# Kernel optimization log

Hardware: AMD Instinct MI355X
Metric: run time of the kernel (lower is better)

## Reference

```python
import jax, jax.numpy as jnp
import numpy as np

B, S, H, NH = 2, 2048, 768, 12
HD = H // NH  # 64
MAXPOS = 2048


def _rope_tables(max_pos, d):
    # bert4torch get_sinusoid_encoding_table: even cols sin, odd cols cos
    pos = np.arange(max_pos, dtype=np.float32)[:, None]
    div = np.exp(np.arange(0, d, 2, dtype=np.float32) * (-np.log(10000.0) / d))
    tab = np.zeros((max_pos, d), np.float32)
    tab[:, 0::2] = np.sin(pos * div)
    tab[:, 1::2] = np.cos(pos * div)
    cos = np.concatenate([tab[:, 1::2], tab[:, 1::2]], axis=1)  # [:,1::2].repeat(1,2)
    sin = np.concatenate([tab[:, 0::2], tab[:, 0::2]], axis=1)  # [:,0::2].repeat(1,2)
    return jnp.asarray(cos), jnp.asarray(sin)


def setup_inputs() -> dict:
    key = jax.random.key(0)
    ks = jax.random.split(key, 10)
    s = 0.02
    inp = {}
    inp["hidden_states"] = jax.random.normal(ks[0], (B, S, H), jnp.float32)
    inp["attention_mask"] = jnp.ones((B, 1, 1, S), jnp.float32)
    for i, n in enumerate(["q", "k", "v", "o"]):
        inp[f"W{n}"] = (jax.random.normal(ks[1 + i], (H, H), jnp.float32) * s)
        inp[f"b{n}"] = jnp.zeros((H,), jnp.float32)
    cos, sin = _rope_tables(MAXPOS, HD)
    inp["cos_position"] = cos
    inp["sin_position"] = sin
    return inp


def _apply_rope(qw, cos, sin):
    # Faithful to source: seq_len_dim defaults to 1, which on a
    # [B, heads, S, head_dim] tensor is the HEADS axis.
    L = qw.shape[1]
    qw2 = jnp.concatenate([-qw[..., 1::2], qw[..., 0::2]], axis=-1)
    return qw * cos[:L][None, :, None, :] + qw2 * sin[:L][None, :, None, :]


def reference(hidden_states, attention_mask, Wq, bq, Wk, bk, Wv, bv, Wo, bo,
              cos_position, sin_position):
    b, s, _ = hidden_states.shape

    def heads(x):  # [b,s,H] -> [b,NH,s,HD]
        return x.reshape(b, s, NH, HD).transpose(0, 2, 1, 3)

    q = heads(hidden_states @ Wq + bq)
    k = heads(hidden_states @ Wk + bk)
    v = heads(hidden_states @ Wv + bv)
    q = _apply_rope(q, cos_position, sin_position)
    k = _apply_rope(k, cos_position, sin_position)
    scores = jnp.einsum('bnid,bnjd->bnij', q, k) / jnp.sqrt(jnp.float32(HD))
    scores = scores + (1.0 - attention_mask) * (-10000.0)
    probs = jax.nn.softmax(scores, axis=-1)  # dropout is identity in eval
    ctx = jnp.einsum('bnij,bnjd->bnid', probs, v)
    ctx = ctx.transpose(0, 2, 1, 3).reshape(b, s, H)
    return ctx @ Wo + bo
```

## Files before the change

kernel.cpp:

```cpp
#include <hip/hip_runtime.h>

#define B 2
#define S 2048
#define H 768
#define NH 12
#define HD 64
#define BS (B * S)
#define LOG2E 1.4426950408889634f

typedef unsigned short u16;
typedef short short8 __attribute__((ext_vector_type(8)));
typedef float f32x4 __attribute__((ext_vector_type(4)));
typedef float f32x16 __attribute__((ext_vector_type(16)));

__device__ __forceinline__ u16 f2bf(float f) {
    union { float f; unsigned u; } c; c.f = f;
    unsigned u = c.u + 0x7FFFu + ((c.u >> 16) & 1u);
    return (u16)(u >> 16);
}
__device__ __forceinline__ float bf2f(u16 h) {
    union { unsigned u; float f; } c; c.u = ((unsigned)h) << 16;
    return c.f;
}
__device__ __forceinline__ f32x16 zero16() {
    f32x16 v;
    #pragma unroll
    for (int i = 0; i < 16; ++i) v[i] = 0.f;
    return v;
}

__device__ __forceinline__ void g2l16(const u16* g, u16* l) {
    __builtin_amdgcn_global_load_lds(
        (const __attribute__((address_space(1))) void*)g,
        (__attribute__((address_space(3))) void*)l, 16, 0, 0);
}

__global__ __launch_bounds__(256) void prep_hs_kernel(
    const float* __restrict__ src, u16* __restrict__ dst)
{
    size_t i = ((size_t)blockIdx.x * 256 + threadIdx.x) * 8;
    float4 a = *(const float4*)(src + i);
    float4 b = *(const float4*)(src + i + 4);
    short8 p;
    p[0] = (short)f2bf(a.x); p[1] = (short)f2bf(a.y);
    p[2] = (short)f2bf(a.z); p[3] = (short)f2bf(a.w);
    p[4] = (short)f2bf(b.x); p[5] = (short)f2bf(b.y);
    p[6] = (short)f2bf(b.z); p[7] = (short)f2bf(b.w);
    *(short8*)(dst + i) = p;
}

__global__ __launch_bounds__(256) void prep_w_kernel(
    const float* __restrict__ Wq, const float* __restrict__ Wk,
    const float* __restrict__ Wv, const float* __restrict__ Wo,
    u16* __restrict__ WTqkv, u16* __restrict__ WTo)
{
    __shared__ float Lt[64 * 65];
    const int t = threadIdx.x;
    const int z = blockIdx.z;
    const float* W = (z == 0) ? Wq : (z == 1) ? Wk : (z == 2) ? Wv : Wo;
    u16* D = (z == 3) ? WTo : (WTqkv + (size_t)z * H * H);
    const int k0 = blockIdx.x * 64, n0 = blockIdx.y * 64;

    #pragma unroll
    for (int u = 0; u < 4; ++u) {
        int f = t + u * 256;
        int r = f >> 4, c4 = (f & 15) * 4;
        float4 w = *(const float4*)(W + (size_t)(k0 + r) * H + n0 + c4);
        Lt[r * 65 + c4 + 0] = w.x; Lt[r * 65 + c4 + 1] = w.y;
        Lt[r * 65 + c4 + 2] = w.z; Lt[r * 65 + c4 + 3] = w.w;
    }
    __syncthreads();
    #pragma unroll
    for (int u = 0; u < 4; ++u) {
        int f = t + u * 256;
        int n = f >> 4, k4 = (f & 15) * 4;
        ushort4 p;
        p.x = f2bf(Lt[(k4 + 0) * 65 + n]);
        p.y = f2bf(Lt[(k4 + 1) * 65 + n]);
        p.z = f2bf(Lt[(k4 + 2) * 65 + n]);
        p.w = f2bf(Lt[(k4 + 3) * 65 + n]);
        *(ushort4*)(D + (size_t)(n0 + n) * H + k0 + k4) = p;
    }
}

__global__ __launch_bounds__(256) void gemm_qkv_kernel(
    const u16* __restrict__ A, const u16* __restrict__ BT,
    const float* __restrict__ bq, const float* __restrict__ bk,
    const float* __restrict__ bv,
    u16* __restrict__ Qb, u16* __restrict__ Kb, u16* __restrict__ VT)
{
    __shared__ alignas(16) u16 As[128 * 72];
    __shared__ alignas(16) u16 Bs[128 * 72];

    const int tid  = threadIdx.x;
    const int w    = tid >> 6;
    const int lane = tid & 63;
    const int quad = lane >> 4;
    const int l15  = lane & 15;
    const int wm = (w & 1) * 64, wn = (w >> 1) * 64;
    const int m0 = blockIdx.x * 128;
    const int n0 = blockIdx.y * 128;
    const int lr = tid >> 3, lc8 = (tid & 7) * 8;

    f32x4 acc[4][4];
    #pragma unroll
    for (int i = 0; i < 4; ++i)
        #pragma unroll
        for (int j = 0; j < 4; ++j) acc[i][j] = (f32x4){0.f, 0.f, 0.f, 0.f};

    short8 pa[2], pb[2], pa2[2], pb2[2];
    #pragma unroll
    for (int u = 0; u < 2; ++u) {
        pa[u]  = *(const short8*)(A  + (size_t)(m0 + lr + u * 32) * H + lc8);
        pb[u]  = *(const short8*)(BT + (size_t)(n0 + lr + u * 32) * H + lc8);
        pa2[u] = *(const short8*)(A  + (size_t)(m0 + lr + 64 + u * 32) * H + lc8);
        pb2[u] = *(const short8*)(BT + (size_t)(n0 + lr + 64 + u * 32) * H + lc8);
    }

    for (int k0 = 0; k0 < H; k0 += 64) {
        __syncthreads();
        #pragma unroll
        for (int u = 0; u < 2; ++u) {
            *(short8*)&As[(lr + u * 32) * 72 + lc8] = pa[u];
            *(short8*)&Bs[(lr + u * 32) * 72 + lc8] = pb[u];
            *(short8*)&As[(lr + 64 + u * 32) * 72 + lc8] = pa2[u];
            *(short8*)&Bs[(lr + 64 + u * 32) * 72 + lc8] = pb2[u];
        }
        if (k0 + 64 < H) {
            #pragma unroll
            for (int u = 0; u < 2; ++u) {
                pa[u]  = *(const short8*)(A  + (size_t)(m0 + lr + u * 32) * H + k0 + 64 + lc8);
                pb[u]  = *(const short8*)(BT + (size_t)(n0 + lr + u * 32) * H + k0 + 64 + lc8);
                pa2[u] = *(const short8*)(A  + (size_t)(m0 + lr + 64 + u * 32) * H + k0 + 64 + lc8);
                pb2[u] = *(const short8*)(BT + (size_t)(n0 + lr + 64 + u * 32) * H + k0 + 64 + lc8);
            }
        }
        __syncthreads();
        #pragma unroll
        for (int kc = 0; kc < 64; kc += 32) {
            short8 af[4], bf[4];
            #pragma unroll
            for (int mi = 0; mi < 4; ++mi)
                af[mi] = *(const short8*)&As[(wm + mi * 16 + l15) * 72 + kc + quad * 8];
            #pragma unroll
            for (int ni = 0; ni < 4; ++ni)
                bf[ni] = *(const short8*)&Bs[(wn + ni * 16 + l15) * 72 + kc + quad * 8];
            #pragma unroll
            for (int mi = 0; mi < 4; ++mi)
                #pragma unroll
                for (int ni = 0; ni < 4; ++ni)
                    acc[mi][ni] = __builtin_amdgcn_mfma_f32_16x16x32_bf16(
                        af[mi], bf[ni], acc[mi][ni], 0, 0, 0);
        }
    }

    #pragma unroll
    for (int mi = 0; mi < 4; ++mi) {
        const int mbase = m0 + wm + mi * 16 + quad * 4;
        #pragma unroll
        for (int ni = 0; ni < 4; ++ni) {
            const int col = n0 + wn + ni * 16 + l15;
            const int which = col / H;
            const int c = col - which * H;
            const int h = c >> 6, d = c & 63;
            if (which == 2) {
                const float bias = bv[c];
                const int b_ = mbase >> 11, s = mbase & (S - 1);
                ushort4 pk;
                pk.x = f2bf(acc[mi][ni][0] + bias);
                pk.y = f2bf(acc[mi][ni][1] + bias);
                pk.z = f2bf(acc[mi][ni][2] + bias);
                pk.w = f2bf(acc[mi][ni][3] + bias);
                *(ushort4*)&VT[(((size_t)b_ * NH + h) * HD + d) * S + s] = pk;
            } else {
                u16* dst = (which == 0) ? Qb : Kb;
                const float bias = (which == 0) ? bq[c] : bk[c];
                #pragma unroll
                for (int r = 0; r < 4; ++r) {
                    int m = mbase + r;
                    int b_ = m >> 11, s = m & (S - 1);
                    dst[(((size_t)b_ * NH + h) * S + s) * HD + d] =
                        f2bf(acc[mi][ni][r] + bias);
                }
            }
        }
    }
}

__global__ __launch_bounds__(256) void gemm_out_kernel(
    const u16* __restrict__ A, const u16* __restrict__ BT,
    const float* __restrict__ bo, float* __restrict__ out)
{
    __shared__ alignas(16) u16 As[128 * 72];
    __shared__ alignas(16) u16 Bs[64 * 72];

    const int tid  = threadIdx.x;
    const int w    = tid >> 6;
    const int lane = tid & 63;
    const int quad = lane >> 4;
    const int l15  = lane & 15;
    const int wm = (w & 1) * 64, wn = (w >> 1) * 32;
    const int m0 = blockIdx.x * 128;
    const int n0 = blockIdx.y * 64;
    const int lr = tid >> 3, lc8 = (tid & 7) * 8;

    f32x4 acc[4][2];
    #pragma unroll
    for (int i = 0; i < 4; ++i)
        #pragma unroll
        for (int j = 0; j < 2; ++j) acc[i][j] = (f32x4){0.f, 0.f, 0.f, 0.f};

    short8 pa[2], pa2[2], pb[2];
    #pragma unroll
    for (int u = 0; u < 2; ++u) {
        pa[u]  = *(const short8*)(A  + (size_t)(m0 + lr + u * 32) * H + lc8);
        pa2[u] = *(const short8*)(A  + (size_t)(m0 + lr + 64 + u * 32) * H + lc8);
        pb[u]  = *(const short8*)(BT + (size_t)(n0 + lr + u * 32) * H + lc8);
    }

    for (int k0 = 0; k0 < H; k0 += 64) {
        __syncthreads();
        #pragma unroll
        for (int u = 0; u < 2; ++u) {
            *(short8*)&As[(lr + u * 32) * 72 + lc8] = pa[u];
            *(short8*)&As[(lr + 64 + u * 32) * 72 + lc8] = pa2[u];
            *(short8*)&Bs[(lr + u * 32) * 72 + lc8] = pb[u];
        }
        if (k0 + 64 < H) {
            #pragma unroll
            for (int u = 0; u < 2; ++u) {
                pa[u]  = *(const short8*)(A  + (size_t)(m0 + lr + u * 32) * H + k0 + 64 + lc8);
                pa2[u] = *(const short8*)(A  + (size_t)(m0 + lr + 64 + u * 32) * H + k0 + 64 + lc8);
                pb[u]  = *(const short8*)(BT + (size_t)(n0 + lr + u * 32) * H + k0 + 64 + lc8);
            }
        }
        __syncthreads();
        #pragma unroll
        for (int kc = 0; kc < 64; kc += 32) {
            short8 af[4], bf[2];
            #pragma unroll
            for (int mi = 0; mi < 4; ++mi)
                af[mi] = *(const short8*)&As[(wm + mi * 16 + l15) * 72 + kc + quad * 8];
            #pragma unroll
            for (int ni = 0; ni < 2; ++ni)
                bf[ni] = *(const short8*)&Bs[(wn + ni * 16 + l15) * 72 + kc + quad * 8];
            #pragma unroll
            for (int mi = 0; mi < 4; ++mi)
                #pragma unroll
                for (int ni = 0; ni < 2; ++ni)
                    acc[mi][ni] = __builtin_amdgcn_mfma_f32_16x16x32_bf16(
                        af[mi], bf[ni], acc[mi][ni], 0, 0, 0);
        }
    }

    #pragma unroll
    for (int mi = 0; mi < 4; ++mi) {
        const int mbase = m0 + wm + mi * 16 + quad * 4;
        #pragma unroll
        for (int ni = 0; ni < 2; ++ni) {
            const int col = n0 + wn + ni * 16 + l15;
            const float bias = bo[col];
            #pragma unroll
            for (int r = 0; r < 4; ++r)
                out[(size_t)(mbase + r) * H + col] = acc[mi][ni][r] + bias;
        }
    }
}

__global__ __launch_bounds__(256) void rope_kernel(
    u16* __restrict__ Qb, u16* __restrict__ Kb,
    const float* __restrict__ cosp, const float* __restrict__ sinp)
{
    int row  = blockIdx.x * 4 + (threadIdx.x >> 6);
    int lane = threadIdx.x & 63;
    u16* X = (blockIdx.y == 0) ? Qb : Kb;
    const float scale = (blockIdx.y == 0) ? (0.125f * LOG2E) : 1.0f;
    int n = (row / S) % NH;
    float x = bf2f(X[(size_t)row * HD + lane]);
    int p = (lane < 32) ? (2 * lane + 1) : (2 * (lane - 32));
    float xp = __shfl(x, p, 64);
    float x2 = (lane < 32) ? -xp : xp;
    float c  = cosp[n * HD + lane];
    float sn = sinp[n * HD + lane];
    X[(size_t)row * HD + lane] = f2bf(fmaf(x, c, x2 * sn) * scale);
}

__global__ __launch_bounds__(256) void attn_mfma_kernel(
    const u16* __restrict__ Q, const u16* __restrict__ K,
    const u16* __restrict__ VT, const float* __restrict__ mask,
    u16* __restrict__ ctx)
{
    __shared__ alignas(16) u16 smem[21504];
    u16* const Kbase = smem;
    u16* const Vbase = smem + 8192;
    u16* const Psw   = smem + 16384 + (threadIdx.x >> 6) * 1280;

    const int tid  = threadIdx.x;
    const int w    = tid >> 6;
    const int lane = tid & 63;
    const int l31  = lane & 31;
    const int h5   = lane >> 5;
    const int rh   = w & 1;
    const int kh   = w >> 1;
    const int bn = blockIdx.y, b = bn / NH, hh = bn % NH;
    const int q0 = blockIdx.x * 64;
    const int NT = S / 64;

    short8 qa[4];
    {
        const u16* Qp = Q + ((size_t)bn * S + q0 + rh * 32 + l31) * HD + h5 * 8;
        #pragma unroll
        for (int kc = 0; kc < 4; ++kc)
            qa[kc] = *(const short8*)(Qp + kc * 16);
    }

    const u16* Kg = K + (size_t)bn * S * HD;
    const u16* Vg = VT + (size_t)bn * HD * S;
    const float* mrow = mask + (size_t)b * S;

    int srow[2], slc[2];
    #pragma unroll
    for (int u = 0; u < 2; ++u) {
        int s = u * 256 + tid;
        srow[u] = s >> 3;
        slc[u]  = (s & 7) ^ (srow[u] & 7);
    }

    #define STAGE(JT, NB)                                                     \
        _Pragma("unroll")                                                     \
        for (int u = 0; u < 2; ++u) {                                         \
            g2l16(Kg + (size_t)((JT) * 64 + srow[u]) * HD + slc[u] * 8,       \
                  Kbase + (NB) * 4096 + (u * 256 + w * 64) * 8);              \
            g2l16(Vg + (size_t)srow[u] * S + (JT) * 64 + slc[u] * 8,          \
                  Vbase + (NB) * 4096 + (u * 256 + w * 64) * 8);              \
        }

    STAGE(0, 0)

    f32x16 o0 = zero16(), o1 = zero16();
    float l_p[16];
    #pragma unroll
    for (int i = 0; i < 16; ++i) l_p[i] = 0.f;

    for (int jt = 0; jt < NT; ++jt) {
        const int cur = jt & 1;
        const float mv = mrow[jt * 64 + kh * 32 + l31];
        __syncthreads();
        if (jt + 1 < NT) { STAGE(jt + 1, cur ^ 1) }

        const u16* Kc = Kbase + cur * 4096;
        const u16* Vc = Vbase + cur * 4096;

        f32x16 sc = zero16();
        {
            const int krow = kh * 32 + l31;
            const int sw = krow & 7;
            #pragma unroll
            for (int kc = 0; kc < 4; ++kc) {
                const short8 kb =
                    *(const short8*)&Kc[krow * 64 + ((kc * 2 + h5) ^ sw) * 8];
                sc = __builtin_amdgcn_mfma_f32_32x32x16_bf16(qa[kc], kb, sc, 0, 0, 0);
            }
        }

        const float mt = (1.0f - mv) * (-10000.0f * LOG2E);
        #pragma unroll
        for (int reg = 0; reg < 16; ++reg) {
            float p = __builtin_amdgcn_exp2f(sc[reg] + mt);
            l_p[reg] += p;
            const int r32 = (reg & 3) + 8 * (reg >> 2) + 4 * h5;
            Psw[r32 * 40 + l31] = f2bf(p);
        }

        asm volatile("s_waitcnt lgkmcnt(0)" ::: "memory");

        const short8 pa0 = *(const short8*)&Psw[l31 * 40 + h5 * 8];
        const short8 pa1 = *(const short8*)&Psw[l31 * 40 + 16 + h5 * 8];

        #pragma unroll
        for (int nt = 0; nt < 2; ++nt) {
            const int vrow = nt * 32 + l31;
            const int sw = vrow & 7;
            const short8 vb0 =
                *(const short8*)&Vc[vrow * 64 + ((kh * 4 + h5) ^ sw) * 8];
            const short8 vb1 =
                *(const short8*)&Vc[vrow * 64 + ((kh * 4 + 2 + h5) ^ sw) * 8];
            f32x16& o = nt ? o1 : o0;
            o = __builtin_amdgcn_mfma_f32_32x32x16_bf16(pa0, vb0, o, 0, 0, 0);
            o = __builtin_amdgcn_mfma_f32_32x32x16_bf16(pa1, vb1, o, 0, 0, 0);
        }
    }
    #undef STAGE

    #pragma unroll
    for (int reg = 0; reg < 16; ++reg) {
        #pragma unroll
        for (int off = 16; off >= 1; off >>= 1)
            l_p[reg] += __shfl_xor(l_p[reg], off, 32);
    }

    __syncthreads();
    float* cb = (float*)smem;
    float* lb = (float*)(smem + 16384);

    if (kh == 1) {
        float* c = cb + rh * 2048;
        #pragma unroll
        for (int reg = 0; reg < 16; ++reg) {
            float2 v = make_float2(o0[reg], o1[reg]);
            *(float2*)&c[reg * 128 + lane * 2] = v;
        }
        if (l31 == 0) {
            #pragma unroll
            for (int reg = 0; reg < 16; ++reg)
                lb[rh * 32 + h5 * 16 + reg] = l_p[reg];
        }
    }
    __syncthreads();
    if (kh == 0) {
        const float* c = cb + rh * 2048;
        #pragma unroll
        for (int reg = 0; reg < 16; ++reg) {
            float2 po = *(const float2*)&c[reg * 128 + lane * 2];
            float lt = l_p[reg] + lb[rh * 32 + h5 * 16 + reg];
            float inv = 1.0f / lt;
            const int r32 = (reg & 3) + 8 * (reg >> 2) + 4 * h5;
            const int s = q0 + rh * 32 + r32;
            u16* dst = ctx + ((size_t)b * S + s) * H + hh * 64;
            dst[l31]      = f2bf((o0[reg] + po.x) * inv);
            dst[32 + l31] = f2bf((o1[reg] + po.y) * inv);
        }
    }
}

extern "C" void kernel_launch(void* const* d_in, const int* in_sizes, int n_in,
                              void* d_out, int out_size, void* d_ws, size_t ws_size,
                              hipStream_t stream)
{
    const float* hs   = (const float*)d_in[0];
    const float* mask = (const float*)d_in[1];
    const float* Wq   = (const float*)d_in[2];
    const float* bq   = (const float*)d_in[3];
    const float* Wk   = (const float*)d_in[4];
    const float* bk   = (const float*)d_in[5];
    const float* Wv   = (const float*)d_in[6];
    const float* bv   = (const float*)d_in[7];
    const float* Wo   = (const float*)d_in[8];
    const float* bo   = (const float*)d_in[9];
    const float* cosp = (const float*)d_in[10];
    const float* sinp = (const float*)d_in[11];
    float* out = (float*)d_out;

    const size_t per = (size_t)B * NH * S * HD;
    u16* ws    = (u16*)d_ws;
    u16* hsb   = ws;
    u16* WTqkv = hsb + per;
    u16* WTo   = WTqkv + (size_t)3 * H * H;
    u16* Qb    = WTo + (size_t)H * H;
    u16* Kb    = Qb + per;
    u16* VT    = Kb + per;
    u16* ctxb  = VT + per;

    prep_hs_kernel<<<(BS * H) / 2048, 256, 0, stream>>>(hs, hsb);
    prep_w_kernel<<<dim3(12, 12, 4), 256, 0, stream>>>(
        Wq, Wk, Wv, Wo, WTqkv, WTo);

    gemm_qkv_kernel<<<dim3(BS / 128, 2304 / 128), 256, 0, stream>>>(
        hsb, WTqkv, bq, bk, bv, Qb, Kb, VT);

    rope_kernel<<<dim3(B * NH * S / 4, 2), 256, 0, stream>>>(
        Qb, Kb, cosp, sinp);

    attn_mfma_kernel<<<dim3(S / 64, B * NH), 256, 0, stream>>>(
        Qb, Kb, VT, mask, ctxb);

    gemm_out_kernel<<<dim3(BS / 128, H / 64), 256, 0, stream>>>(
        ctxb, WTo, bo, out);
}
```

Before: 200.9 us.

## Fold RoPE and scale into Q/K weights and use direct global-to-LDS loads

Because RoPE here rotates along the head axis, it acts as a fixed per-head linear map on the feature dimension. The change therefore applies it, together with the softmax scale, to the transposed Q/K weights and biases inside the weight-prep kernel, and drops the separate rope kernel along with its read-modify-write pass over Q and K. The QKV GEMM also switches from register-staged prefetch to direct global-to-LDS loads (g2l16) into an XOR-swizzled, unpadded shared layout. This loses the explicit register double-buffering, and folding the rotation into the weights before bf16 rounding changes rounding slightly.

```diff
diff --git a/kernel.cpp b/kernel.cpp
--- a/kernel.cpp
+++ b/kernel.cpp
@@ -52,7 +52,10 @@
 __global__ __launch_bounds__(256) void prep_w_kernel(
     const float* __restrict__ Wq, const float* __restrict__ Wk,
     const float* __restrict__ Wv, const float* __restrict__ Wo,
-    u16* __restrict__ WTqkv, u16* __restrict__ WTo)
+    const float* __restrict__ bq, const float* __restrict__ bk,
+    const float* __restrict__ cosp, const float* __restrict__ sinp,
+    u16* __restrict__ WTqkv, u16* __restrict__ WTo,
+    float* __restrict__ bqk2)
 {
     __shared__ float Lt[64 * 65];
     const int t = threadIdx.x;
@@ -60,6 +63,17 @@
     const float* W = (z == 0) ? Wq : (z == 1) ? Wk : (z == 2) ? Wv : Wo;
     u16* D = (z == 3) ? WTo : (WTqkv + (size_t)z * H * H);
     const int k0 = blockIdx.x * 64, n0 = blockIdx.y * 64;
+    const int head = n0 >> 6;
+    const float scl = (z == 0) ? (0.125f * LOG2E) : 1.0f;
+
+    if (z < 2 && blockIdx.x == 0 && t < 64) {
+        const float* bs = (z == 0) ? bq : bk;
+        int d = t;
+        int pd = (d < 32) ? (2 * d + 1) : (2 * (d - 32));
+        float sv = ((d < 32) ? -1.f : 1.f) * sinp[head * HD + d];
+        float cv = cosp[head * HD + d];
+        bqk2[z * H + n0 + d] = scl * (cv * bs[n0 + d] + sv * bs[n0 + pd]);
+    }
 
     #pragma unroll
     for (int u = 0; u < 4; ++u) {
@@ -75,22 +89,31 @@
         int f = t + u * 256;
         int n = f >> 4, k4 = (f & 15) * 4;
         ushort4 p;
-        p.x = f2bf(Lt[(k4 + 0) * 65 + n]);
-        p.y = f2bf(Lt[(k4 + 1) * 65 + n]);
-        p.z = f2bf(Lt[(k4 + 2) * 65 + n]);
-        p.w = f2bf(Lt[(k4 + 3) * 65 + n]);
+        if (z < 2) {
+            int pn = (n < 32) ? (2 * n + 1) : (2 * (n - 32));
+            float cv = scl * cosp[head * HD + n];
+            float sv = scl * ((n < 32) ? -1.f : 1.f) * sinp[head * HD + n];
+            p.x = f2bf(cv * Lt[(k4 + 0) * 65 + n] + sv * Lt[(k4 + 0) * 65 + pn]);
+            p.y = f2bf(cv * Lt[(k4 + 1) * 65 + n] + sv * Lt[(k4 + 1) * 65 + pn]);
+            p.z = f2bf(cv * Lt[(k4 + 2) * 65 + n] + sv * Lt[(k4 + 2) * 65 + pn]);
+            p.w = f2bf(cv * Lt[(k4 + 3) * 65 + n] + sv * Lt[(k4 + 3) * 65 + pn]);
+        } else {
+            p.x = f2bf(Lt[(k4 + 0) * 65 + n]);
+            p.y = f2bf(Lt[(k4 + 1) * 65 + n]);
+            p.z = f2bf(Lt[(k4 + 2) * 65 + n]);
+            p.w = f2bf(Lt[(k4 + 3) * 65 + n]);
+        }
         *(ushort4*)(D + (size_t)(n0 + n) * H + k0 + k4) = p;
     }
 }
 
 __global__ __launch_bounds__(256) void gemm_qkv_kernel(
     const u16* __restrict__ A, const u16* __restrict__ BT,
-    const float* __restrict__ bq, const float* __restrict__ bk,
-    const float* __restrict__ bv,
+    const float* __restrict__ bqk2, const float* __restrict__ bv,
     u16* __restrict__ Qb, u16* __restrict__ Kb, u16* __restrict__ VT)
 {
-    __shared__ alignas(16) u16 As[128 * 72];
-    __shared__ alignas(16) u16 Bs[128 * 72];
+    __shared__ alignas(16) u16 As[128 * 64];
+    __shared__ alignas(16) u16 Bs[128 * 64];
 
     const int tid  = threadIdx.x;
     const int w    = tid >> 6;
@@ -100,51 +123,45 @@
     const int wm = (w & 1) * 64, wn = (w >> 1) * 64;
     const int m0 = blockIdx.x * 128;
     const int n0 = blockIdx.y * 128;
-    const int lr = tid >> 3, lc8 = (tid & 7) * 8;
+
+    int srow[4], slc[4];
+    #pragma unroll
+    for (int u = 0; u < 4; ++u) {
+        int s = u * 256 + tid;
+        srow[u] = s >> 3;
+        slc[u]  = (s & 7) ^ (srow[u] & 7);
+    }
 
     f32x4 acc[4][4];
     #pragma unroll
     for (int i = 0; i < 4; ++i)
         #pragma unroll
         for (int j = 0; j < 4; ++j) acc[i][j] = (f32x4){0.f, 0.f, 0.f, 0.f};
-
-    short8 pa[2], pb[2], pa2[2], pb2[2];
-    #pragma unroll
-    for (int u = 0; u < 2; ++u) {
-        pa[u]  = *(const short8*)(A  + (size_t)(m0 + lr + u * 32) * H + lc8);
-        pb[u]  = *(const short8*)(BT + (size_t)(n0 + lr + u * 32) * H + lc8);
-        pa2[u] = *(const short8*)(A  + (size_t)(m0 + lr + 64 + u * 32) * H + lc8);
-        pb2[u] = *(const short8*)(BT + (size_t)(n0 + lr + 64 + u * 32) * H + lc8);
-    }
 
     for (int k0 = 0; k0 < H; k0 += 64) {
         __syncthreads();
         #pragma unroll
-        for (int u = 0; u < 2; ++u) {
-            *(short8*)&As[(lr + u * 32) * 72 + lc8] = pa[u];
-            *(short8*)&Bs[(lr + u * 32) * 72 + lc8] = pb[u];
-            *(short8*)&As[(lr + 64 + u * 32) * 72 + lc8] = pa2[u];
-            *(short8*)&Bs[(lr + 64 + u * 32) * 72 + lc8] = pb2[u];
-        }
-        if (k0 + 64 < H) {
-            #pragma unroll
-            for (int u = 0; u < 2; ++u) {
-                pa[u]  = *(const short8*)(A  + (size_t)(m0 + lr + u * 32) * H + k0 + 64 + lc8);
-                pb[u]  = *(const short8*)(BT + (size_t)(n0 + lr + u * 32) * H + k0 + 64 + lc8);
-                pa2[u] = *(const short8*)(A  + (size_t)(m0 + lr + 64 + u * 32) * H + k0 + 64 + lc8);
-                pb2[u] = *(const short8*)(BT + (size_t)(n0 + lr + 64 + u * 32) * H + k0 + 64 + lc8);
+        for (int u = 0; u < 4; ++u) {
+            g2l16(A  + (size_t)(m0 + srow[u]) * H + k0 + slc[u] * 8,
+                  As + (u * 256 + w * 64) * 8);
+            g2l16(BT + (size_t)(n0 + srow[u]) * H + k0 + slc[u] * 8,
+                  Bs + (u * 256 + w * 64) * 8);
+        }
+        __syncthreads();
+        #pragma unroll
+        for (int kc = 0; kc < 2; ++kc) {
+            const int ch = kc * 4 + quad;
+            short8 af[4], bf[4];
+            #pragma unroll
+            for (int mi = 0; mi < 4; ++mi) {
+                int row = wm + mi * 16 + l15;
+                af[mi] = *(const short8*)&As[row * 64 + (ch ^ (row & 7)) * 8];
             }
-        }
-        __syncthreads();
-        #pragma unroll
-        for (int kc = 0; kc < 64; kc += 32) {
-            short8 af[4], bf[4];
-            #pragma unroll
-            for (int mi = 0; mi < 4; ++mi)
-                af[mi] = *(const short8*)&As[(wm + mi * 16 + l15) * 72 + kc + quad * 8];
-            #pragma unroll
-            for (int ni = 0; ni < 4; ++ni)
-                bf[ni] = *(const short8*)&Bs[(wn + ni * 16 + l15) * 72 + kc + quad * 8];
+            #pragma unroll
+            for (int ni = 0; ni < 4; ++ni) {
+                int row = wn + ni * 16 + l15;
+                bf[ni] = *(const short8*)&Bs[row * 64 + (ch ^ (row & 7)) * 8];
+            }
             #pragma unroll
             for (int mi = 0; mi < 4; ++mi)
                 #pragma unroll
@@ -174,7 +191,7 @@
                 *(ushort4*)&VT[(((size_t)b_ * NH + h) * HD + d) * S + s] = pk;
             } else {
                 u16* dst = (which == 0) ? Qb : Kb;
-                const float bias = (which == 0) ? bq[c] : bk[c];
+                const float bias = bqk2[which * H + c];
                 #pragma unroll
                 for (int r = 0; r < 4; ++r) {
                     int m = mbase + r;
@@ -265,24 +282,6 @@
                 out[(size_t)(mbase + r) * H + col] = acc[mi][ni][r] + bias;
         }
     }
-}
-
-__global__ __launch_bounds__(256) void rope_kernel(
-    u16* __restrict__ Qb, u16* __restrict__ Kb,
-    const float* __restrict__ cosp, const float* __restrict__ sinp)
-{
-    int row  = blockIdx.x * 4 + (threadIdx.x >> 6);
-    int lane = threadIdx.x & 63;
-    u16* X = (blockIdx.y == 0) ? Qb : Kb;
-    const float scale = (blockIdx.y == 0) ? (0.125f * LOG2E) : 1.0f;
-    int n = (row / S) % NH;
-    float x = bf2f(X[(size_t)row * HD + lane]);
-    int p = (lane < 32) ? (2 * lane + 1) : (2 * (lane - 32));
-    float xp = __shfl(x, p, 64);
-    float x2 = (lane < 32) ? -xp : xp;
-    float c  = cosp[n * HD + lane];
-    float sn = sinp[n * HD + lane];
-    X[(size_t)row * HD + lane] = f2bf(fmaf(x, c, x2 * sn) * scale);
 }
 
 __global__ __launch_bounds__(256) void attn_mfma_kernel(
@@ -460,16 +459,14 @@
     u16* Kb    = Qb + per;
     u16* VT    = Kb + per;
     u16* ctxb  = VT + per;
+    float* bqk2 = (float*)(ctxb + per);
 
     prep_hs_kernel<<<(BS * H) / 2048, 256, 0, stream>>>(hs, hsb);
     prep_w_kernel<<<dim3(12, 12, 4), 256, 0, stream>>>(
-        Wq, Wk, Wv, Wo, WTqkv, WTo);
+        Wq, Wk, Wv, Wo, bq, bk, cosp, sinp, WTqkv, WTo, bqk2);
 
     gemm_qkv_kernel<<<dim3(BS / 128, 2304 / 128), 256, 0, stream>>>(
-        hsb, WTqkv, bq, bk, bv, Qb, Kb, VT);
-
-    rope_kernel<<<dim3(B * NH * S / 4, 2), 256, 0, stream>>>(
-        Qb, Kb, cosp, sinp);
+        hsb, WTqkv, bqk2, bv, Qb, Kb, VT);
 
     attn_mfma_kernel<<<dim3(S / 64, B * NH), 256, 0, stream>>>(
         Qb, Kb, VT, mask, ctxb);
```

After: 195.8 us. -2.6%, faster.
